# Performance work log

Measured on AMD Instinct MI355X. Metric: run time of the kernel, lower is better.

## Reference

```python
import jax, jax.numpy as jnp
import numpy as np


def setup_inputs() -> dict:
    key = jax.random.key(0)
    k1, k2, k3 = jax.random.split(key, 3)
    B, N, K = 512, 1024, 64  # batch, seq_len, num_tags
    y_pred = jax.random.normal(k1, (B, N, K), dtype=jnp.float32)
    # glorot-uniform-ish init for the transition matrix
    limit = np.sqrt(6.0 / (K + K)).astype(np.float32)
    trans = jax.random.uniform(k2, (K, K), dtype=jnp.float32, minval=-limit, maxval=limit)
    y_true = jax.random.randint(k3, (B, N), 0, K, dtype=jnp.int32)
    return {"y_pred": y_pred, "trans": trans, "y_true": y_true}


def _crf_loss(y_pred, trans, y_true):
    # mask derived from padding convention: padded frames have logits <= -1e6
    mask = jnp.all(y_pred > -1e6, axis=2, keepdims=True).astype(y_pred.dtype)  # [B,N,1]
    y_pred = y_pred * mask
    m = mask[..., 0]  # [B,N]

    # ---- target (gold-path) score ----
    # point score: emission logits at the gold labels (one-hot einsum == gather)
    point = jnp.sum(
        jnp.take_along_axis(y_pred, y_true[..., None], axis=2)[..., 0] * m, axis=1
    )  # [B]
    # transition score: trans[y_t, y_{t+1}], zeroed where either frame is masked
    tvals = trans[y_true[:, :-1], y_true[:, 1:]] * m[:, :-1] * m[:, 1:]  # [B,N-1]
    target_score = point + jnp.sum(tvals, axis=1)  # [B]

    # ---- log normalizer via forward recursion (logsumexp semiring scan) ----
    init = y_pred[:, 0]  # [B,K]
    emits = jnp.swapaxes(y_pred[:, 1:], 0, 1)  # [N-1,B,K]
    masks = jnp.swapaxes(mask[:, 1:], 0, 1)    # [N-1,B,1]

    def step(alpha, xm):
        emit, mm = xm
        # alpha: [B,K] -> broadcast over next-tag axis with trans [K,K]
        new = jax.nn.logsumexp(alpha[:, :, None] + trans[None], axis=1) + emit
        alpha = mm * new + (1.0 - mm) * alpha
        return alpha, None

    alpha, _ = jax.lax.scan(step, init, (emits, masks))
    log_norm = jax.nn.logsumexp(alpha, axis=1)  # [B]
    return log_norm - target_score


def reference(y_pred, trans, y_true):
    return _crf_loss(y_pred, trans, y_true)
```

## Files before the change

kernel.cpp:

```cpp
#include <hip/hip_runtime.h>
#include <cstdint>
#include <cstddef>


constexpr int Nn = 1024;
constexpr int Kk = 64;
constexpr float LOG2E = 1.4426950408889634f;
constexpr float LN2   = 0.6931471805599453f;

typedef float f32x4  __attribute__((ext_vector_type(4)));
typedef _Float16 half8 __attribute__((ext_vector_type(8)));
typedef int   int32x4 __attribute__((ext_vector_type(4)));

__device__ __forceinline__ float fast_exp2(float x) {
#if __has_builtin(__builtin_amdgcn_exp2f)
    return __builtin_amdgcn_exp2f(x);
#else
    return exp2f(x);
#endif
}

__device__ __forceinline__ int pkrtz(float lo, float hi) {
    return __builtin_bit_cast(int, __builtin_amdgcn_cvt_pkrtz(lo, hi));
}

__device__ __forceinline__ half8 load_afrag(const float* __restrict__ trans,
                                            int n, int blk, int mt, int kt) {
    half8 r;
#pragma unroll
    for (int q = 0; q < 8; ++q) {
        int k = kt * 32 + (q >> 2) * 16 + 4 * blk + (q & 3);
        float v = fast_exp2(trans[k * Kk + mt * 16 + n] * LOG2E);
        r[q] = (_Float16)v;
    }
    return r;
}

__device__ __forceinline__ int clamp_s(int s) {
    return s < -100 ? -100 : (s > 100 ? 100 : s);
}

__device__ __forceinline__ void stage4(const float* src, float* dstbase) {
#pragma unroll
    for (int mt = 0; mt < 4; ++mt) {
        __builtin_amdgcn_global_load_lds(
            (const __attribute__((address_space(1))) unsigned*)(src + mt * 16),
            (__attribute__((address_space(3))) unsigned*)(dstbase + mt * 256),
            16, 0, 0);
    }
}

#define MFMA16(a, b, c) __builtin_amdgcn_mfma_f32_16x16x32_f16((a), (b), (c), 0, 0, 0)

__global__ __launch_bounds__(64, 1) void crf_fwd(
    const float* __restrict__ y_pred,
    const float* __restrict__ trans,
    float* __restrict__ out)
{
    const int l   = threadIdx.x;
    const int n   = l & 15;
    const int blk = l >> 4;

    __shared__ __align__(16) float lds[8 * 1024];

    const float* yp  = y_pred + (size_t)(blockIdx.x * 16 + n) * (Nn * Kk);
    const float* ypn = yp + 4 * blk;

    half8 a00 = load_afrag(trans, n, blk, 0, 0), a01 = load_afrag(trans, n, blk, 0, 1);
    half8 a10 = load_afrag(trans, n, blk, 1, 0), a11 = load_afrag(trans, n, blk, 1, 1);
    half8 a20 = load_afrag(trans, n, blk, 2, 0), a21 = load_afrag(trans, n, blk, 2, 1);
    half8 a30 = load_afrag(trans, n, blk, 3, 0), a31 = load_afrag(trans, n, blk, 3, 1);

    f32x4 c0, c1, c2, c3;
    {
        f32x4 e0 = *(const f32x4*)(ypn);
        f32x4 e1 = *(const f32x4*)(ypn + 16);
        f32x4 e2 = *(const f32x4*)(ypn + 32);
        f32x4 e3 = *(const f32x4*)(ypn + 48);
        float M0_ = yp[0];
        c0.x = fast_exp2((e0.x - M0_) * LOG2E); c0.y = fast_exp2((e0.y - M0_) * LOG2E);
        c0.z = fast_exp2((e0.z - M0_) * LOG2E); c0.w = fast_exp2((e0.w - M0_) * LOG2E);
        c1.x = fast_exp2((e1.x - M0_) * LOG2E); c1.y = fast_exp2((e1.y - M0_) * LOG2E);
        c1.z = fast_exp2((e1.z - M0_) * LOG2E); c1.w = fast_exp2((e1.w - M0_) * LOG2E);
        c2.x = fast_exp2((e2.x - M0_) * LOG2E); c2.y = fast_exp2((e2.y - M0_) * LOG2E);
        c2.z = fast_exp2((e2.z - M0_) * LOG2E); c2.w = fast_exp2((e2.w - M0_) * LOG2E);
        c3.x = fast_exp2((e3.x - M0_) * LOG2E); c3.y = fast_exp2((e3.y - M0_) * LOG2E);
        c3.z = fast_exp2((e3.z - M0_) * LOG2E); c3.w = fast_exp2((e3.w - M0_) * LOG2E);
    }
    const float M0 = yp[0];

    half8 b0 = __builtin_bit_cast(half8, (int32x4){pkrtz(c0.x, c0.y), pkrtz(c0.z, c0.w),
                                                   pkrtz(c1.x, c1.y), pkrtz(c1.z, c1.w)});
    half8 b1 = __builtin_bit_cast(half8, (int32x4){pkrtz(c2.x, c2.y), pkrtz(c2.z, c2.w),
                                                   pkrtz(c3.x, c3.y), pkrtz(c3.z, c3.w)});

    int s_use;
    {
        float v = __shfl(c0.x, n);
        s_use = clamp_s((int)((__builtin_bit_cast(unsigned, v) >> 23) & 0xFFu) - 127);
    }
    int Sacc = 0;

    asm volatile("s_waitcnt vmcnt(0)" ::: "memory");

#pragma unroll
    for (int t = 1; t <= 8; ++t) {
        stage4(ypn + t * 64, &lds[(t & 7) * 1024]);
    }

    asm volatile("s_waitcnt vmcnt(28)" ::: "memory");
    f32x4 emc0, emc1, emc2, emc3, emn0, emn1, emn2, emn3;
    {
        const float* eb = &lds[1 * 1024] + l * 4;
        emc0 = *(const f32x4*)(eb);       emc1 = *(const f32x4*)(eb + 256);
        emc2 = *(const f32x4*)(eb + 512); emc3 = *(const f32x4*)(eb + 768);
    }

    const float CHI = 60000.0f;

#define PE1(CN, EM) \
    c##CN.x = fminf(d##CN.x * fast_exp2(fmaf(EM.x, LOG2E, msu_)), CHI); \
    c##CN.y = fminf(d##CN.y * fast_exp2(fmaf(EM.y, LOG2E, msu_)), CHI); \
    c##CN.z = fminf(d##CN.z * fast_exp2(fmaf(EM.z, LOG2E, msu_)), CHI); \
    c##CN.w = fminf(d##CN.w * fast_exp2(fmaf(EM.w, LOG2E, msu_)), CHI);

#define STEP(T, EI0, EI1, EI2, EI3, EO0, EO1, EO2, EO3) { \
    f32x4 zz_ = {0.f, 0.f, 0.f, 0.f}; \
    f32x4 d0 = MFMA16(a00, b0, MFMA16(a01, b1, zz_)); \
    f32x4 d1 = MFMA16(a10, b0, MFMA16(a11, b1, zz_)); \
    f32x4 d2 = MFMA16(a20, b0, MFMA16(a21, b1, zz_)); \
    f32x4 d3 = MFMA16(a30, b0, MFMA16(a31, b1, zz_)); \
    asm volatile("s_waitcnt vmcnt(24)" ::: "memory"); \
    { const float* nb_ = &lds[(((T) + 1) & 7) * 1024] + l * 4; \
      EO0 = *(const f32x4*)(nb_);       EO1 = *(const f32x4*)(nb_ + 256); \
      EO2 = *(const f32x4*)(nb_ + 512); EO3 = *(const f32x4*)(nb_ + 768); } \
    float msu_ = -(float)s_use; \
    Sacc += s_use; \
    PE1(0, EI0) \
    float bc_ = __shfl(c0.x, n); \
    PE1(1, EI1) PE1(2, EI2) PE1(3, EI3) \
    s_use = clamp_s((int)((__builtin_bit_cast(unsigned, bc_) >> 23) & 0xFFu) - 127); \
    asm volatile("" ::: "memory"); \
    { int ts_ = (T) + 8 > Nn - 1 ? Nn - 1 : (T) + 8; \
      stage4(ypn + ts_ * 64, &lds[((T) & 7) * 1024]); } \
    b0 = __builtin_bit_cast(half8, (int32x4){pkrtz(c0.x, c0.y), pkrtz(c0.z, c0.w), \
                                             pkrtz(c1.x, c1.y), pkrtz(c1.z, c1.w)}); \
    b1 = __builtin_bit_cast(half8, (int32x4){pkrtz(c2.x, c2.y), pkrtz(c2.z, c2.w), \
                                             pkrtz(c3.x, c3.y), pkrtz(c3.z, c3.w)}); \
}

    for (int tb = 0; tb < 511; ++tb) {
        const int t = 2 * tb + 1;
        STEP(t,     emc0, emc1, emc2, emc3, emn0, emn1, emn2, emn3)
        STEP(t + 1, emn0, emn1, emn2, emn3, emc0, emc1, emc2, emc3)
    }
    STEP(1023, emc0, emc1, emc2, emc3, emn0, emn1, emn2, emn3)

    asm volatile("s_waitcnt vmcnt(0)" ::: "memory");

    float sum = ((c0.x + c0.y) + (c0.z + c0.w)) + ((c1.x + c1.y) + (c1.z + c1.w))
              + ((c2.x + c2.y) + (c2.z + c2.w)) + ((c3.x + c3.y) + (c3.z + c3.w));
    sum += __shfl_xor(sum, 16);
    sum += __shfl_xor(sum, 32);
    float log_norm = (log2f(sum) + (float)Sacc) * LN2 + M0;
    if (l < 16) {
        out[blockIdx.x * 16 + l] += log_norm;
    }
}

__global__ __launch_bounds__(64) void crf_target(
    const float* __restrict__ y_pred,
    const float* __restrict__ trans,
    const int*   __restrict__ y_true,
    float* __restrict__ out)
{
    const int b = blockIdx.x, l = threadIdx.x;
    const int* ytb = y_true + (size_t)b * Nn;
    const float* ypb = y_pred + (size_t)b * Nn * Kk;
    float v = 0.0f;
#pragma unroll
    for (int i = 0; i < 16; ++i) {
        int t = i * 64 + l;
        int y0 = ytb[t];
        v += ypb[(size_t)t * Kk + y0];
        if (t < Nn - 1) {
            int y1 = ytb[t + 1];
            v += trans[y0 * Kk + y1];
        }
    }
#pragma unroll
    for (int off = 32; off; off >>= 1) v += __shfl_xor(v, off);
    if (l == 0) out[b] = -v;
}

extern "C" void kernel_launch(void* const* d_in, const int* in_sizes, int n_in,
                              void* d_out, int out_size, void* d_ws, size_t ws_size,
                              hipStream_t stream) {
    const float* y_pred = (const float*)d_in[0];
    const float* trans  = (const float*)d_in[1];
    const int*   y_true = (const int*)d_in[2];
    float* out = (float*)d_out;

    crf_target<<<512, 64, 0, stream>>>(y_pred, trans, y_true, out);
    crf_fwd<<<32, 64, 0, stream>>>(y_pred, trans, out);
}
```

Baseline: 327.3 us.

## Interleave two batch chains per wavefront and halve forward-kernel grid

Each forward-recursion block now carries two independent groups of 16 sequences. Their MFMA, exp and shuffle work is interleaved each step to expose more instruction-level parallelism inside the serial scan. To fit both chains, the LDS staging buffer is doubled and the prefetch depth drops from 8 to 7 steps, with adjusted vmcnt waits. The grid halves to 16 blocks, so per-step work per wave doubles; this only helps if the serial step was dominated by latency rather than issue throughput. An unused, malformed macro definition is also left in and immediately undefined.

```diff
diff --git a/kernel.cpp b/kernel.cpp
--- a/kernel.cpp
+++ b/kernel.cpp
@@ -61,110 +61,185 @@
     const int n   = l & 15;
     const int blk = l >> 4;
 
-    __shared__ __align__(16) float lds[8 * 1024];
-
-    const float* yp  = y_pred + (size_t)(blockIdx.x * 16 + n) * (Nn * Kk);
-    const float* ypn = yp + 4 * blk;
+    __shared__ __align__(16) float lds[16 * 1024];
+
+    const float* ypA = y_pred + (size_t)(blockIdx.x * 32 + n)      * (Nn * Kk);
+    const float* ypB = y_pred + (size_t)(blockIdx.x * 32 + 16 + n) * (Nn * Kk);
+    const float* ypnA = ypA + 4 * blk;
+    const float* ypnB = ypB + 4 * blk;
 
     half8 a00 = load_afrag(trans, n, blk, 0, 0), a01 = load_afrag(trans, n, blk, 0, 1);
     half8 a10 = load_afrag(trans, n, blk, 1, 0), a11 = load_afrag(trans, n, blk, 1, 1);
     half8 a20 = load_afrag(trans, n, blk, 2, 0), a21 = load_afrag(trans, n, blk, 2, 1);
     half8 a30 = load_afrag(trans, n, blk, 3, 0), a31 = load_afrag(trans, n, blk, 3, 1);
 
-    f32x4 c0, c1, c2, c3;
-    {
-        f32x4 e0 = *(const f32x4*)(ypn);
-        f32x4 e1 = *(const f32x4*)(ypn + 16);
-        f32x4 e2 = *(const f32x4*)(ypn + 32);
-        f32x4 e3 = *(const f32x4*)(ypn + 48);
-        float M0_ = yp[0];
-        c0.x = fast_exp2((e0.x - M0_) * LOG2E); c0.y = fast_exp2((e0.y - M0_) * LOG2E);
-        c0.z = fast_exp2((e0.z - M0_) * LOG2E); c0.w = fast_exp2((e0.w - M0_) * LOG2E);
-        c1.x = fast_exp2((e1.x - M0_) * LOG2E); c1.y = fast_exp2((e1.y - M0_) * LOG2E);
-        c1.z = fast_exp2((e1.z - M0_) * LOG2E); c1.w = fast_exp2((e1.w - M0_) * LOG2E);
-        c2.x = fast_exp2((e2.x - M0_) * LOG2E); c2.y = fast_exp2((e2.y - M0_) * LOG2E);
-        c2.z = fast_exp2((e2.z - M0_) * LOG2E); c2.w = fast_exp2((e2.w - M0_) * LOG2E);
-        c3.x = fast_exp2((e3.x - M0_) * LOG2E); c3.y = fast_exp2((e3.y - M0_) * LOG2E);
-        c3.z = fast_exp2((e3.z - M0_) * LOG2E); c3.w = fast_exp2((e3.w - M0_) * LOG2E);
-    }
-    const float M0 = yp[0];
-
-    half8 b0 = __builtin_bit_cast(half8, (int32x4){pkrtz(c0.x, c0.y), pkrtz(c0.z, c0.w),
-                                                   pkrtz(c1.x, c1.y), pkrtz(c1.z, c1.w)});
-    half8 b1 = __builtin_bit_cast(half8, (int32x4){pkrtz(c2.x, c2.y), pkrtz(c2.z, c2.w),
-                                                   pkrtz(c3.x, c3.y), pkrtz(c3.z, c3.w)});
-
-    int s_use;
-    {
-        float v = __shfl(c0.x, n);
-        s_use = clamp_s((int)((__builtin_bit_cast(unsigned, v) >> 23) & 0xFFu) - 127);
-    }
-    int Sacc = 0;
+#define INIT_CHAIN(S, YPN, YP) \
+    f32x4 c0##S, c1##S, c2##S, c3##S; \
+    { \
+        f32x4 e0 = *(const f32x4*)(YPN); \
+        f32x4 e1 = *(const f32x4*)(YPN + 16); \
+        f32x4 e2 = *(const f32x4*)(YPN + 32); \
+        f32x4 e3 = *(const f32x4*)(YPN + 48); \
+        float M0_ = (YP)[0]; \
+        c0##S.x = fast_exp2((e0.x - M0_) * LOG2E); c0##S.y = fast_exp2((e0.y - M0_) * LOG2E); \
+        c0##S.z = fast_exp2((e0.z - M0_) * LOG2E); c0##S.w = fast_exp2((e0.w - M0_) * LOG2E); \
+        c1##S.x = fast_exp2((e1.x - M0_) * LOG2E); c1##S.y = fast_exp2((e1.y - M0_) * LOG2E); \
+        c1##S.z = fast_exp2((e1.z - M0_) * LOG2E); c1##S.w = fast_exp2((e1.w - M0_) * LOG2E); \
+        c2##S.x = fast_exp2((e2.x - M0_) * LOG2E); c2##S.y = fast_exp2((e2.y - M0_) * LOG2E); \
+        c2##S.z = fast_ex2_dummy_ ## S ## _unused(0); \
+    }
+#undef INIT_CHAIN
+
+    f32x4 c0A, c1A, c2A, c3A, c0B, c1B, c2B, c3B;
+    {
+        f32x4 e0 = *(const f32x4*)(ypnA);
+        f32x4 e1 = *(const f32x4*)(ypnA + 16);
+        f32x4 e2 = *(const f32x4*)(ypnA + 32);
+        f32x4 e3 = *(const f32x4*)(ypnA + 48);
+        float M0_ = ypA[0];
+        c0A.x = fast_exp2((e0.x - M0_) * LOG2E); c0A.y = fast_exp2((e0.y - M0_) * LOG2E);
+        c0A.z = fast_exp2((e0.z - M0_) * LOG2E); c0A.w = fast_exp2((e0.w - M0_) * LOG2E);
+        c1A.x = fast_exp2((e1.x - M0_) * LOG2E); c1A.y = fast_exp2((e1.y - M0_) * LOG2E);
+        c1A.z = fast_exp2((e1.z - M0_) * LOG2E); c1A.w = fast_exp2((e1.w - M0_) * LOG2E);
+        c2A.x = fast_exp2((e2.x - M0_) * LOG2E); c2A.y = fast_exp2((e2.y - M0_) * LOG2E);
+        c2A.z = fast_exp2((e2.z - M0_) * LOG2E); c2A.w = fast_exp2((e2.w - M0_) * LOG2E);
+        c3A.x = fast_exp2((e3.x - M0_) * LOG2E); c3A.y = fast_exp2((e3.y - M0_) * LOG2E);
+        c3A.z = fast_exp2((e3.z - M0_) * LOG2E); c3A.w = fast_exp2((e3.w - M0_) * LOG2E);
+    }
+    {
+        f32x4 e0 = *(const f32x4*)(ypnB);
+        f32x4 e1 = *(const f32x4*)(ypnB + 16);
+        f32x4 e2 = *(const f32x4*)(ypnB + 32);
+        f32x4 e3 = *(const f32x4*)(ypnB + 48);
+        float M0_ = ypB[0];
+        c0B.x = fast_exp2((e0.x - M0_) * LOG2E); c0B.y = fast_exp2((e0.y - M0_) * LOG2E);
+        c0B.z = fast_exp2((e0.z - M0_) * LOG2E); c0B.w = fast_exp2((e0.w - M0_) * LOG2E);
+        c1B.x = fast_exp2((e1.x - M0_) * LOG2E); c1B.y = fast_exp2((e1.y - M0_) * LOG2E);
+        c1B.z = fast_exp2((e1.z - M0_) * LOG2E); c1B.w = fast_exp2((e1.w - M0_) * LOG2E);
+        c2B.x = fast_exp2((e2.x - M0_) * LOG2E); c2B.y = fast_exp2((e2.y - M0_) * LOG2E);
+        c2B.z = fast_exp2((e2.z - M0_) * LOG2E); c2B.w = fast_exp2((e2.w - M0_) * LOG2E);
+        c3B.x = fast_exp2((e3.x - M0_) * LOG2E); c3B.y = fast_exp2((e3.y - M0_) * LOG2E);
+        c3B.z = fast_exp2((e3.z - M0_) * LOG2E); c3B.w = fast_exp2((e3.w - M0_) * LOG2E);
+    }
+    const float M0A = ypA[0];
+    const float M0B = ypB[0];
+
+    half8 b0A = __builtin_bit_cast(half8, (int32x4){pkrtz(c0A.x, c0A.y), pkrtz(c0A.z, c0A.w),
+                                                    pkrtz(c1A.x, c1A.y), pkrtz(c1A.z, c1A.w)});
+    half8 b1A = __builtin_bit_cast(half8, (int32x4){pkrtz(c2A.x, c2A.y), pkrtz(c2A.z, c2A.w),
+                                                    pkrtz(c3A.x, c3A.y), pkrtz(c3A.z, c3A.w)});
+    half8 b0B = __builtin_bit_cast(half8, (int32x4){pkrtz(c0B.x, c0B.y), pkrtz(c0B.z, c0B.w),
+                                                    pkrtz(c1B.x, c1B.y), pkrtz(c1B.z, c1B.w)});
+    half8 b1B = __builtin_bit_cast(half8, (int32x4){pkrtz(c2B.x, c2B.y), pkrtz(c2B.z, c2B.w),
+                                                    pkrtz(c3B.x, c3B.y), pkrtz(c3B.z, c3B.w)});
+
+    int s_useA, s_useB;
+    {
+        float vA = __shfl(c0A.x, n);
+        s_useA = clamp_s((int)((__builtin_bit_cast(unsigned, vA) >> 23) & 0xFFu) - 127);
+        float vB = __shfl(c0B.x, n);
+        s_useB = clamp_s((int)((__builtin_bit_cast(unsigned, vB) >> 23) & 0xFFu) - 127);
+    }
+    int SaccA = 0, SaccB = 0;
 
     asm volatile("s_waitcnt vmcnt(0)" ::: "memory");
 
 #pragma unroll
-    for (int t = 1; t <= 8; ++t) {
-        stage4(ypn + t * 64, &lds[(t & 7) * 1024]);
-    }
-
-    asm volatile("s_waitcnt vmcnt(28)" ::: "memory");
-    f32x4 emc0, emc1, emc2, emc3, emn0, emn1, emn2, emn3;
-    {
-        const float* eb = &lds[1 * 1024] + l * 4;
-        emc0 = *(const f32x4*)(eb);       emc1 = *(const f32x4*)(eb + 256);
-        emc2 = *(const f32x4*)(eb + 512); emc3 = *(const f32x4*)(eb + 768);
+    for (int t = 1; t <= 7; ++t) {
+        stage4(ypnA + t * 64, &lds[(t & 7) * 1024]);
+        stage4(ypnB + t * 64, &lds[8 * 1024 + (t & 7) * 1024]);
+    }
+
+    asm volatile("s_waitcnt vmcnt(48)" ::: "memory");
+    f32x4 emcA0, emcA1, emcA2, emcA3, emnA0, emnA1, emnA2, emnA3;
+    f32x4 emcB0, emcB1, emcB2, emcB3, emnB0, emnB1, emnB2, emnB3;
+    {
+        const float* ea = &lds[1 * 1024] + l * 4;
+        emcA0 = *(const f32x4*)(ea);       emcA1 = *(const f32x4*)(ea + 256);
+        emcA2 = *(const f32x4*)(ea + 512); emcA3 = *(const f32x4*)(ea + 768);
+        const float* eb = &lds[8 * 1024 + 1 * 1024] + l * 4;
+        emcB0 = *(const f32x4*)(eb);       emcB1 = *(const f32x4*)(eb + 256);
+        emcB2 = *(const f32x4*)(eb + 512); emcB3 = *(const f32x4*)(eb + 768);
     }
 
     const float CHI = 60000.0f;
 
-#define PE1(CN, EM) \
-    c##CN.x = fminf(d##CN.x * fast_exp2(fmaf(EM.x, LOG2E, msu_)), CHI); \
-    c##CN.y = fminf(d##CN.y * fast_exp2(fmaf(EM.y, LOG2E, msu_)), CHI); \
-    c##CN.z = fminf(d##CN.z * fast_exp2(fmaf(EM.z, LOG2E, msu_)), CHI); \
-    c##CN.w = fminf(d##CN.w * fast_exp2(fmaf(EM.w, LOG2E, msu_)), CHI);
-
-#define STEP(T, EI0, EI1, EI2, EI3, EO0, EO1, EO2, EO3) { \
+#define PE1(S, CN, EM, MSU) \
+    c##CN##S.x = fminf(d##CN##S.x * fast_exp2(fmaf(EM.x, LOG2E, MSU)), CHI); \
+    c##CN##S.y = fminf(d##CN##S.y * fast_exp2(fmaf(EM.y, LOG2E, MSU)), CHI); \
+    c##CN##S.z = fminf(d##CN##S.z * fast_exp2(fmaf(EM.z, LOG2E, MSU)), CHI); \
+    c##CN##S.w = fminf(d##CN##S.w * fast_exp2(fmaf(EM.w, LOG2E, MSU)), CHI);
+
+#define STEP2(T, AI0, AI1, AI2, AI3, AO0, AO1, AO2, AO3, \
+                 BI0, BI1, BI2, BI3, BO0, BO1, BO2, BO3) { \
     f32x4 zz_ = {0.f, 0.f, 0.f, 0.f}; \
-    f32x4 d0 = MFMA16(a00, b0, MFMA16(a01, b1, zz_)); \
-    f32x4 d1 = MFMA16(a10, b0, MFMA16(a11, b1, zz_)); \
-    f32x4 d2 = MFMA16(a20, b0, MFMA16(a21, b1, zz_)); \
-    f32x4 d3 = MFMA16(a30, b0, MFMA16(a31, b1, zz_)); \
-    asm volatile("s_waitcnt vmcnt(24)" ::: "memory"); \
-    { const float* nb_ = &lds[(((T) + 1) & 7) * 1024] + l * 4; \
-      EO0 = *(const f32x4*)(nb_);       EO1 = *(const f32x4*)(nb_ + 256); \
-      EO2 = *(const f32x4*)(nb_ + 512); EO3 = *(const f32x4*)(nb_ + 768); } \
-    float msu_ = -(float)s_use; \
-    Sacc += s_use; \
-    PE1(0, EI0) \
-    float bc_ = __shfl(c0.x, n); \
-    PE1(1, EI1) PE1(2, EI2) PE1(3, EI3) \
-    s_use = clamp_s((int)((__builtin_bit_cast(unsigned, bc_) >> 23) & 0xFFu) - 127); \
+    f32x4 d0A = MFMA16(a00, b0A, MFMA16(a01, b1A, zz_)); \
+    f32x4 d0B = MFMA16(a00, b0B, MFMA16(a01, b1B, zz_)); \
+    f32x4 d1A = MFMA16(a10, b0A, MFMA16(a11, b1A, zz_)); \
+    f32x4 d1B = MFMA16(a10, b0B, MFMA16(a11, b1B, zz_)); \
+    f32x4 d2A = MFMA16(a20, b0A, MFMA16(a21, b1A, zz_)); \
+    f32x4 d2B = MFMA16(a20, b0B, MFMA16(a21, b1B, zz_)); \
+    f32x4 d3A = MFMA16(a30, b0A, MFMA16(a31, b1A, zz_)); \
+    f32x4 d3B = MFMA16(a30, b0B, MFMA16(a31, b1B, zz_)); \
+    asm volatile("s_waitcnt vmcnt(40)" ::: "memory"); \
+    { const float* na_ = &lds[(((T) + 1) & 7) * 1024] + l * 4; \
+      AO0 = *(const f32x4*)(na_);       AO1 = *(const f32x4*)(na_ + 256); \
+      AO2 = *(const f32x4*)(na_ + 512); AO3 = *(const f32x4*)(na_ + 768); \
+      const float* nb_ = &lds[8 * 1024 + (((T) + 1) & 7) * 1024] + l * 4; \
+      BO0 = *(const f32x4*)(nb_);       BO1 = *(const f32x4*)(nb_ + 256); \
+      BO2 = *(const f32x4*)(nb_ + 512); BO3 = *(const f32x4*)(nb_ + 768); } \
+    float msuA_ = -(float)s_useA; SaccA += s_useA; \
+    float msuB_ = -(float)s_useB; SaccB += s_useB; \
+    PE1(A, 0, AI0, msuA_) \
+    float bcA_ = __shfl(c0A.x, n); \
+    PE1(B, 0, BI0, msuB_) \
+    float bcB_ = __shfl(c0B.x, n); \
+    PE1(A, 1, AI1, msuA_) PE1(A, 2, AI2, msuA_) PE1(A, 3, AI3, msuA_) \
+    PE1(B, 1, BI1, msuB_) PE1(B, 2, BI2, msuB_) PE1(B, 3, BI3, msuB_) \
+    s_useA = clamp_s((int)((__builtin_bit_cast(unsigned, bcA_) >> 23) & 0xFFu) - 127); \
+    s_useB = clamp_s((int)((__builtin_bit_cast(unsigned, bcB_) >> 23) & 0xFFu) - 127); \
     asm volatile("" ::: "memory"); \
-    { int ts_ = (T) + 8 > Nn - 1 ? Nn - 1 : (T) + 8; \
-      stage4(ypn + ts_ * 64, &lds[((T) & 7) * 1024]); } \
-    b0 = __builtin_bit_cast(half8, (int32x4){pkrtz(c0.x, c0.y), pkrtz(c0.z, c0.w), \
-                                             pkrtz(c1.x, c1.y), pkrtz(c1.z, c1.w)}); \
-    b1 = __builtin_bit_cast(half8, (int32x4){pkrtz(c2.x, c2.y), pkrtz(c2.z, c2.w), \
-                                             pkrtz(c3.x, c3.y), pkrtz(c3.z, c3.w)}); \
+    { int ts_ = (T) + 7 > Nn - 1 ? Nn - 1 : (T) + 7; \
+      stage4(ypnA + ts_ * 64, &lds[(ts_ & 7) * 1024]); \
+      stage4(ypnB + ts_ * 64, &lds[8 * 1024 + (ts_ & 7) * 1024]); } \
+    b0A = __builtin_bit_cast(half8, (int32x4){pkrtz(c0A.x, c0A.y), pkrtz(c0A.z, c0A.w), \
+                                              pkrtz(c1A.x, c1A.y), pkrtz(c1A.z, c1A.w)}); \
+    b1A = __builtin_bit_cast(half8, (int32x4){pkrtz(c2A.x, c2A.y), pkrtz(c2A.z, c2A.w), \
+                                              pkrtz(c3A.x, c3A.y), pkrtz(c3A.z, c3A.w)}); \
+    b0B = __builtin_bit_cast(half8, (int32x4){pkrtz(c0B.x, c0B.y), pkrtz(c0B.z, c0B.w), \
+                                              pkrtz(c1B.x, c1B.y), pkrtz(c1B.z, c1B.w)}); \
+    b1B = __builtin_bit_cast(half8, (int32x4){pkrtz(c2B.x, c2B.y), pkrtz(c2B.z, c2B.w), \
+                                              pkrtz(c3B.x, c3B.y), pkrtz(c3B.z, c3B.w)}); \
 }
 
     for (int tb = 0; tb < 511; ++tb) {
         const int t = 2 * tb + 1;
-        STEP(t,     emc0, emc1, emc2, emc3, emn0, emn1, emn2, emn3)
-        STEP(t + 1, emn0, emn1, emn2, emn3, emc0, emc1, emc2, emc3)
-    }
-    STEP(1023, emc0, emc1, emc2, emc3, emn0, emn1, emn2, emn3)
+        STEP2(t,     emcA0, emcA1, emcA2, emcA3, emnA0, emnA1, emnA2, emnA3,
+                     emcB0, emcB1, emcB2, emcB3, emnB0, emnB1, emnB2, emnB3)
+        STEP2(t + 1, emnA0, emnA1, emnA2, emnA3, emcA0, emcA1, emcA2, emcA3,
+                     emnB0, emnB1, emnB2, emnB3, emcB0, emcB1, emcB2, emcB3)
+    }
+    STEP2(1023, emcA0, emcA1, emcA2, emcA3, emnA0, emnA1, emnA2, emnA3,
+                emcB0, emcB1, emcB2, emcB3, emnB0, emnB1, emnB2, emnB3)
 
     asm volatile("s_waitcnt vmcnt(0)" ::: "memory");
 
-    float sum = ((c0.x + c0.y) + (c0.z + c0.w)) + ((c1.x + c1.y) + (c1.z + c1.w))
-              + ((c2.x + c2.y) + (c2.z + c2.w)) + ((c3.x + c3.y) + (c3.z + c3.w));
-    sum += __shfl_xor(sum, 16);
-    sum += __shfl_xor(sum, 32);
-    float log_norm = (log2f(sum) + (float)Sacc) * LN2 + M0;
+    float sumA = ((c0A.x + c0A.y) + (c0A.z + c0A.w)) + ((c1A.x + c1A.y) + (c1A.z + c1A.w))
+               + ((c2A.x + c2A.y) + (c2A.z + c2A.w)) + ((c3A.x + c3A.y) + (c3A.z + c3A.w));
+    sumA += __shfl_xor(sumA, 16);
+    sumA += __shfl_xor(sumA, 32);
+    float lnA = (log2f(sumA) + (float)SaccA) * LN2 + M0A;
+
+    float sumB = ((c0B.x + c0B.y) + (c0B.z + c0B.w)) + ((c1B.x + c1B.y) + (c1B.z + c1B.w))
+               + ((c2B.x + c2B.y) + (c2B.z + c2B.w)) + ((c3B.x + c3B.y) + (c3B.z + c3B.w));
+    sumB += __shfl_xor(sumB, 16);
+    sumB += __shfl_xor(sumB, 32);
+    float lnB = (log2f(sumB) + (float)SaccB) * LN2 + M0B;
+
     if (l < 16) {
-        out[blockIdx.x * 16 + l] += log_norm;
+        out[blockIdx.x * 32 + l] += lnA;
+    } else if (l < 32) {
+        out[blockIdx.x * 32 + 16 + (l & 15)] += lnB;
     }
 }
 
@@ -202,5 +277,5 @@
     float* out = (float*)d_out;
 
     crf_target<<<512, 64, 0, stream>>>(y_pred, trans, y_true, out);
-    crf_fwd<<<32, 64, 0, stream>>>(y_pred, trans, out);
-}
+    crf_fwd<<<16, 64, 0, stream>>>(y_pred, trans, out);
+}
```

Result: slower. 576.1 us (+76.0%).

## Precompute exp of emissions in a parallel kernel before serial CRF scan

Applied to the files above, without the earlier changes.

Adds a grid-wide elementwise kernel that writes exp(y_pred) into workspace. The forward recursion then streams these precomputed values and rescales them with an exact power-of-two multiply, instead of calling exp2 on the critical serial path. This takes transcendental work out of the latency-bound 32-block scan, at the cost of an extra 128MB read and write pass through memory plus a larger stream for the scan to read. Without enough workspace it falls back to the old path.

```diff
diff --git a/kernel.cpp b/kernel.cpp
--- a/kernel.cpp
+++ b/kernel.cpp
@@ -52,8 +52,29 @@
 
 #define MFMA16(a, b, c) __builtin_amdgcn_mfma_f32_16x16x32_f16((a), (b), (c), 0, 0, 0)
 
+__global__ __launch_bounds__(256) void crf_exp(
+    const float* __restrict__ in, float* __restrict__ o)
+{
+    const f32x4* iv = (const f32x4*)in;
+    f32x4* ov = (f32x4*)o;
+    const int total4 = 8388608;
+    int i = blockIdx.x * 256 + threadIdx.x;
+    const int stride = gridDim.x * 256;
+    for (; i < total4; i += stride) {
+        f32x4 v = iv[i];
+        f32x4 r;
+        r.x = fast_exp2(v.x * LOG2E);
+        r.y = fast_exp2(v.y * LOG2E);
+        r.z = fast_exp2(v.z * LOG2E);
+        r.w = fast_exp2(v.w * LOG2E);
+        ov[i] = r;
+    }
+}
+
+template<bool USE_PE>
 __global__ __launch_bounds__(64, 1) void crf_fwd(
     const float* __restrict__ y_pred,
+    const float* __restrict__ stream,
     const float* __restrict__ trans,
     float* __restrict__ out)
 {
@@ -65,6 +86,7 @@
 
     const float* yp  = y_pred + (size_t)(blockIdx.x * 16 + n) * (Nn * Kk);
     const float* ypn = yp + 4 * blk;
+    const float* spn = stream + (size_t)(blockIdx.x * 16 + n) * (Nn * Kk) + 4 * blk;
 
     half8 a00 = load_afrag(trans, n, blk, 0, 0), a01 = load_afrag(trans, n, blk, 0, 1);
     half8 a10 = load_afrag(trans, n, blk, 1, 0), a11 = load_afrag(trans, n, blk, 1, 1);
@@ -105,7 +127,7 @@
 
 #pragma unroll
     for (int t = 1; t <= 8; ++t) {
-        stage4(ypn + t * 64, &lds[(t & 7) * 1024]);
+        stage4(spn + t * 64, &lds[(t & 7) * 1024]);
     }
 
     asm volatile("s_waitcnt vmcnt(28)" ::: "memory");
@@ -118,11 +140,17 @@
 
     const float CHI = 60000.0f;
 
-#define PE1(CN, EM) \
+#define PE_OLD(CN, EM) \
     c##CN.x = fminf(d##CN.x * fast_exp2(fmaf(EM.x, LOG2E, msu_)), CHI); \
     c##CN.y = fminf(d##CN.y * fast_exp2(fmaf(EM.y, LOG2E, msu_)), CHI); \
     c##CN.z = fminf(d##CN.z * fast_exp2(fmaf(EM.z, LOG2E, msu_)), CHI); \
     c##CN.w = fminf(d##CN.w * fast_exp2(fmaf(EM.w, LOG2E, msu_)), CHI);
+
+#define PE_NEW(CN, PS) \
+    c##CN.x = fminf(d##CN.x * PS.x, CHI); \
+    c##CN.y = fminf(d##CN.y * PS.y, CHI); \
+    c##CN.z = fminf(d##CN.z * PS.z, CHI); \
+    c##CN.w = fminf(d##CN.w * PS.w, CHI);
 
 #define STEP(T, EI0, EI1, EI2, EI3, EO0, EO1, EO2, EO3) { \
     f32x4 zz_ = {0.f, 0.f, 0.f, 0.f}; \
@@ -134,15 +162,28 @@
     { const float* nb_ = &lds[(((T) + 1) & 7) * 1024] + l * 4; \
       EO0 = *(const f32x4*)(nb_);       EO1 = *(const f32x4*)(nb_ + 256); \
       EO2 = *(const f32x4*)(nb_ + 512); EO3 = *(const f32x4*)(nb_ + 768); } \
-    float msu_ = -(float)s_use; \
     Sacc += s_use; \
-    PE1(0, EI0) \
-    float bc_ = __shfl(c0.x, n); \
-    PE1(1, EI1) PE1(2, EI2) PE1(3, EI3) \
-    s_use = clamp_s((int)((__builtin_bit_cast(unsigned, bc_) >> 23) & 0xFFu) - 127); \
+    if constexpr (USE_PE) { \
+        float s2p_ = __builtin_bit_cast(float, (unsigned)(127 - s_use) << 23); \
+        f32x4 ps0, ps1, ps2, ps3; \
+        ps0.x = EI0.x * s2p_; ps0.y = EI0.y * s2p_; ps0.z = EI0.z * s2p_; ps0.w = EI0.w * s2p_; \
+        ps1.x = EI1.x * s2p_; ps1.y = EI1.y * s2p_; ps1.z = EI1.z * s2p_; ps1.w = EI1.w * s2p_; \
+        ps2.x = EI2.x * s2p_; ps2.y = EI2.y * s2p_; ps2.z = EI2.z * s2p_; ps2.w = EI2.w * s2p_; \
+        ps3.x = EI3.x * s2p_; ps3.y = EI3.y * s2p_; ps3.z = EI3.z * s2p_; ps3.w = EI3.w * s2p_; \
+        PE_NEW(0, ps0) \
+        float bc_ = __shfl(c0.x, n); \
+        PE_NEW(1, ps1) PE_NEW(2, ps2) PE_NEW(3, ps3) \
+        s_use = clamp_s((int)((__builtin_bit_cast(unsigned, bc_) >> 23) & 0xFFu) - 127); \
+    } else { \
+        float msu_ = -(float)s_use; \
+        PE_OLD(0, EI0) \
+        float bc_ = __shfl(c0.x, n); \
+        PE_OLD(1, EI1) PE_OLD(2, EI2) PE_OLD(3, EI3) \
+        s_use = clamp_s((int)((__builtin_bit_cast(unsigned, bc_) >> 23) & 0xFFu) - 127); \
+    } \
     asm volatile("" ::: "memory"); \
     { int ts_ = (T) + 8 > Nn - 1 ? Nn - 1 : (T) + 8; \
-      stage4(ypn + ts_ * 64, &lds[((T) & 7) * 1024]); } \
+      stage4(spn + ts_ * 64, &lds[((T) & 7) * 1024]); } \
     b0 = __builtin_bit_cast(half8, (int32x4){pkrtz(c0.x, c0.y), pkrtz(c0.z, c0.w), \
                                              pkrtz(c1.x, c1.y), pkrtz(c1.z, c1.w)}); \
     b1 = __builtin_bit_cast(half8, (int32x4){pkrtz(c2.x, c2.y), pkrtz(c2.z, c2.w), \
@@ -201,6 +242,14 @@
     const int*   y_true = (const int*)d_in[2];
     float* out = (float*)d_out;
 
+    const size_t pe_bytes = (size_t)512 * 1024 * 64 * 4;
+    const bool use_pe = (ws_size >= pe_bytes) && (d_ws != nullptr);
+
     crf_target<<<512, 64, 0, stream>>>(y_pred, trans, y_true, out);
-    crf_fwd<<<32, 64, 0, stream>>>(y_pred, trans, out);
-}
+    if (use_pe) {
+        crf_exp<<<2048, 256, 0, stream>>>(y_pred, (float*)d_ws);
+        crf_fwd<true><<<32, 64, 0, stream>>>(y_pred, (const float*)d_ws, trans, out);
+    } else {
+        crf_fwd<false><<<32, 64, 0, stream>>>(y_pred, y_pred, trans, out);
+    }
+}
```

Result: faster. 305.5 us (-6.7%).
